# Kernel optimization log

Hardware: AMD Instinct MI355X
Metric: run time of the kernel (lower is better)

Reference implementation:

```python
import jax, jax.numpy as jnp
import numpy as np

HIDDEN = 1024
N_HEADS = 16
D_HEAD = HIDDEN // N_HEADS


def _rope(q, k):
    # q, k: [B, H, N, d]; interleaved-pair rotation as in the torch module
    B, H, N, d = q.shape
    inv_freq = 1.0 / (10000.0 ** (jnp.arange(0, d, 2, dtype=jnp.float32) / d))  # [d/2]
    pos = jnp.arange(N, dtype=jnp.float32)
    thetas = pos[:, None] * inv_freq[None, :]            # [N, d/2]
    cos, sin = jnp.cos(thetas), jnp.sin(thetas)

    def rot(x):
        xp = x.reshape(B, H, N, d // 2, 2)
        xx, xy = xp[..., 0], xp[..., 1]
        rx = xx * cos - xy * sin
        ry = xx * sin + xy * cos
        return jnp.stack([rx, ry], axis=-1).reshape(B, H, N, d)

    return rot(q), rot(k)


def setup_inputs() -> dict:
    key = jax.random.key(0)
    ks = jax.random.split(key, 9)
    B, N, Hd = 4, 2048, HIDDEN
    s = 1.0 / np.sqrt(Hd)
    return {
        "x": jax.random.normal(ks[0], (B, N, Hd), jnp.float32),
        "Wq": jax.random.normal(ks[1], (Hd, Hd), jnp.float32) * s,
        "bq": jax.random.normal(ks[2], (Hd,), jnp.float32) * 0.02,
        "Wk": jax.random.normal(ks[3], (Hd, Hd), jnp.float32) * s,
        "bk": jax.random.normal(ks[4], (Hd,), jnp.float32) * 0.02,
        "Wv": jax.random.normal(ks[5], (Hd, Hd), jnp.float32) * s,
        "bv": jax.random.normal(ks[6], (Hd,), jnp.float32) * 0.02,
        "Wo": jax.random.normal(ks[7], (Hd, Hd), jnp.float32) * s,
        "bo": jax.random.normal(ks[8], (Hd,), jnp.float32) * 0.02,
    }


def reference(x, Wq, bq, Wk, bk, Wv, bv, Wo, bo):
    B, N, _ = x.shape
    H, d = N_HEADS, D_HEAD
    # torch nn.Linear: y = x @ W.T + b
    q = (x @ Wq.T + bq).reshape(B, N, H, d).transpose(0, 2, 1, 3)  # [B,H,N,d]
    k = (x @ Wk.T + bk).reshape(B, N, H, d).transpose(0, 2, 1, 3)
    v = (x @ Wv.T + bv).reshape(B, N, H, d).transpose(0, 2, 1, 3)
    q, k = _rope(q, k)
    scores = jnp.einsum("bhnd,bhmd->bhnm", q, k) / jnp.sqrt(jnp.asarray(d, x.dtype))
    attn = jax.nn.softmax(scores, axis=-1)
    out = jnp.einsum("bhnm,bhmd->bhnd", attn, v)
    out = out.transpose(0, 2, 1, 3).reshape(B, N, H * d)
    return out @ Wo.T + bo
```

## Files before the change

### kernel.cpp

```cpp
#include <hip/hip_runtime.h>
#include <cmath>

typedef unsigned short u16;
typedef unsigned int u32;
typedef __bf16 bf16_t;
typedef bf16_t bf16x8 __attribute__((ext_vector_type(8)));
typedef float f32x4 __attribute__((ext_vector_type(4)));
typedef u32 u32x4 __attribute__((ext_vector_type(4)));

#define AS1 __attribute__((address_space(1)))
#define AS3 __attribute__((address_space(3)))

__device__ __forceinline__ void g2l16(const void* g, void* l) {
  __builtin_amdgcn_global_load_lds((const AS1 void*)g, (AS3 void*)l, 16, 0, 0);
}

__device__ __forceinline__ u16 f2b(float f) {
  u32 u = __builtin_bit_cast(u32, f);
  u += 0x7FFFu + ((u >> 16) & 1u);
  return (u16)(u >> 16);
}
__device__ __forceinline__ float b2f(u16 h) {
  u32 u = ((u32)h) << 16;
  return __builtin_bit_cast(float, u);
}

__device__ __forceinline__ float exp2fast(float x) {
#if __has_builtin(__builtin_amdgcn_exp2f)
  return __builtin_amdgcn_exp2f(x);
#else
  return exp2f(x);
#endif
}

__device__ __forceinline__ u32 cvtpk(float lo, float hi) {
  u32 d;
  asm("v_cvt_pk_bf16_f32 %0, %1, %2" : "=v"(d) : "v"(lo), "v"(hi));
  return d;
}

__global__ void mha_f2b_kernel(const float* __restrict__ in, u16* __restrict__ out, int n4) {
  int i = blockIdx.x * blockDim.x + threadIdx.x;
  if (i >= n4) return;
  float4 f = reinterpret_cast<const float4*>(in)[i];
  ushort4 o;
  o.x = f2b(f.x); o.y = f2b(f.y); o.z = f2b(f.z); o.w = f2b(f.w);
  reinterpret_cast<ushort4*>(out)[i] = o;
}

__global__ void mha_f2b4_kernel(const float* __restrict__ a0, const float* __restrict__ a1,
                                const float* __restrict__ a2, const float* __restrict__ a3,
                                u16* __restrict__ o0, u16* __restrict__ o1,
                                u16* __restrict__ o2, u16* __restrict__ o3, int n4) {
  int y = blockIdx.y;
  const float* in = y == 0 ? a0 : y == 1 ? a1 : y == 2 ? a2 : a3;
  u16* out = y == 0 ? o0 : y == 1 ? o1 : y == 2 ? o2 : o3;
  int i = blockIdx.x * blockDim.x + threadIdx.x;
  if (i >= n4) return;
  float4 f = reinterpret_cast<const float4*>(in)[i];
  ushort4 o;
  o.x = f2b(f.x); o.y = f2b(f.y); o.z = f2b(f.z); o.w = f2b(f.w);
  reinterpret_cast<ushort4*>(out)[i] = o;
}

#define BM 128
#define BN 128
#define BK 32

__global__ __launch_bounds__(256) void mha_gemm_bt(
    const u16* __restrict__ A, const u16* __restrict__ Bm,
    const float* __restrict__ bias,
    float* __restrict__ Cf, u16* __restrict__ Cb,
    int M, int N, int K)
{
  __shared__ u16 As[BM * BK];
  __shared__ u16 Bs[BN * BK];
  const int tid = threadIdx.x;
  const int wid = tid >> 6, lane = tid & 63;
  const int r16 = lane & 15, g = lane >> 4;
  const int bm = blockIdx.x * BM, bn = blockIdx.y * BN;
  const int wm = (wid >> 1) * 64, wn = (wid & 1) * 64;

  f32x4 acc[4][4] = {};

  const int srow = tid >> 2;
  const int sbyte = (tid & 3) * 16;

  for (int kt = 0; kt < K; kt += BK) {
#pragma unroll
    for (int p = 0; p < 2; ++p) {
      int ra = p * 64 + srow;
      int csw = (sbyte ^ ((ra & 3) << 4)) >> 1;
      g2l16(A  + (size_t)(bm + ra) * K + kt + csw, (u16*)As + p * 2048 + wid * 512);
      g2l16(Bm + (size_t)(bn + ra) * K + kt + csw, (u16*)Bs + p * 2048 + wid * 512);
    }
    __syncthreads();
    bf16x8 af[4], bfr[4];
#pragma unroll
    for (int mf = 0; mf < 4; ++mf) {
      int rr = wm + mf * 16 + r16;
      af[mf] = *reinterpret_cast<const bf16x8*>(&As[rr * 32 + ((g * 8) ^ ((rr & 3) << 3))]);
    }
#pragma unroll
    for (int nf = 0; nf < 4; ++nf) {
      int rr = wn + nf * 16 + r16;
      bfr[nf] = *reinterpret_cast<const bf16x8*>(&Bs[rr * 32 + ((g * 8) ^ ((rr & 3) << 3))]);
    }
    __builtin_amdgcn_s_setprio(1);
#pragma unroll
    for (int mf = 0; mf < 4; ++mf)
#pragma unroll
      for (int nf = 0; nf < 4; ++nf)
        acc[mf][nf] = __builtin_amdgcn_mfma_f32_16x16x32_bf16(af[mf], bfr[nf], acc[mf][nf], 0, 0, 0);
    __builtin_amdgcn_s_setprio(0);
    __syncthreads();
  }

#pragma unroll
  for (int mf = 0; mf < 4; ++mf)
#pragma unroll
    for (int nf = 0; nf < 4; ++nf) {
      int col = bn + wn + nf * 16 + r16;
      float bv = bias ? bias[col] : 0.f;
#pragma unroll
      for (int r = 0; r < 4; ++r) {
        int rowm = bm + wm + mf * 16 + g * 4 + r;
        float v = acc[mf][nf][r] + bv;
        if (Cf) Cf[(size_t)rowm * N + col] = v;
        else    Cb[(size_t)rowm * N + col] = f2b(v);
      }
    }
}

__global__ __launch_bounds__(256) void mha_gemm_qkv(
    const u16* __restrict__ A,
    const u16* __restrict__ W0, const u16* __restrict__ W1, const u16* __restrict__ W2,
    const float* __restrict__ b0, const float* __restrict__ b1, const float* __restrict__ b2,
    u16* __restrict__ C0, u16* __restrict__ C1, u16* __restrict__ C2,
    int M, int N, int K)
{
  __shared__ u16 As[BM * BK];
  __shared__ u16 Bs[BN * BK];
  const int tid = threadIdx.x;
  const int wid = tid >> 6, lane = tid & 63;
  const int r16 = lane & 15, g = lane >> 4;
  const int by = blockIdx.y;
  const int wsel = by >> 3;
  const u16* Bm = wsel == 0 ? W0 : (wsel == 1 ? W1 : W2);
  const float* bias = wsel == 0 ? b0 : (wsel == 1 ? b1 : b2);
  u16* Cb = wsel == 0 ? C0 : (wsel == 1 ? C1 : C2);
  const int bm = blockIdx.x * BM, bn = (by & 7) * BN;
  const int wm = (wid >> 1) * 64, wn = (wid & 1) * 64;

  f32x4 acc[4][4] = {};

  const int srow = tid >> 2;
  const int sbyte = (tid & 3) * 16;

  for (int kt = 0; kt < K; kt += BK) {
#pragma unroll
    for (int p = 0; p < 2; ++p) {
      int ra = p * 64 + srow;
      int csw = (sbyte ^ ((ra & 3) << 4)) >> 1;
      g2l16(A  + (size_t)(bm + ra) * K + kt + csw, (u16*)As + p * 2048 + wid * 512);
      g2l16(Bm + (size_t)(bn + ra) * K + kt + csw, (u16*)Bs + p * 2048 + wid * 512);
    }
    __syncthreads();
    bf16x8 af[4], bfr[4];
#pragma unroll
    for (int mf = 0; mf < 4; ++mf) {
      int rr = wm + mf * 16 + r16;
      af[mf] = *reinterpret_cast<const bf16x8*>(&As[rr * 32 + ((g * 8) ^ ((rr & 3) << 3))]);
    }
#pragma unroll
    for (int nf = 0; nf < 4; ++nf) {
      int rr = wn + nf * 16 + r16;
      bfr[nf] = *reinterpret_cast<const bf16x8*>(&Bs[rr * 32 + ((g * 8) ^ ((rr & 3) << 3))]);
    }
    __builtin_amdgcn_s_setprio(1);
#pragma unroll
    for (int mf = 0; mf < 4; ++mf)
#pragma unroll
      for (int nf = 0; nf < 4; ++nf)
        acc[mf][nf] = __builtin_amdgcn_mfma_f32_16x16x32_bf16(af[mf], bfr[nf], acc[mf][nf], 0, 0, 0);
    __builtin_amdgcn_s_setprio(0);
    __syncthreads();
  }

#pragma unroll
  for (int mf = 0; mf < 4; ++mf)
#pragma unroll
    for (int nf = 0; nf < 4; ++nf) {
      int col = bn + wn + nf * 16 + r16;
      float bv = bias[col];
#pragma unroll
      for (int r = 0; r < 4; ++r) {
        int rowm = bm + wm + mf * 16 + g * 4 + r;
        Cb[(size_t)rowm * N + col] = f2b(acc[mf][nf][r] + bv);
      }
    }
}

__global__ void mha_rope_kernel(u16* __restrict__ Q, u16* __restrict__ Kt) {
  int idx = blockIdx.x * blockDim.x + threadIdx.x;
  u16* P = blockIdx.y ? Kt : Q;
  int rowp = idx >> 9;
  int pc = idx & 511;
  int n = rowp & 2047;
  int j = pc & 31;
  float inv = exp2f(-(float)j * 0.41524101186092503f);
  float th = (float)n * inv;
  float s, c;
  sincosf(th, &s, &c);
  u32* p32 = reinterpret_cast<u32*>(P + (size_t)rowp * 1024 + pc * 2);
  u32 v = *p32;
  float x = b2f((u16)(v & 0xFFFFu));
  float y = b2f((u16)(v >> 16));
  float rx = x * c - y * s;
  float ry = x * s + y * c;
  *p32 = (u32)f2b(rx) | ((u32)f2b(ry) << 16);
}

__global__ void mha_vtrans_kernel(const u16* __restrict__ V, u16* __restrict__ Vt) {
  __shared__ u16 t[64][65];
  const int bh = blockIdx.y;
  const int b = bh >> 4, h = bh & 15;
  const int n0 = blockIdx.x * 64;
  const int tid = threadIdx.x;
#pragma unroll
  for (int i = 0; i < 2; ++i) {
    int rr = i * 32 + (tid >> 3);
    int c8 = (tid & 7) * 8;
    uint4 w = *reinterpret_cast<const uint4*>(V + (size_t)(b * 2048 + n0 + rr) * 1024 + h * 64 + c8);
    t[rr][c8 + 0] = (u16)(w.x & 0xFFFFu); t[rr][c8 + 1] = (u16)(w.x >> 16);
    t[rr][c8 + 2] = (u16)(w.y & 0xFFFFu); t[rr][c8 + 3] = (u16)(w.y >> 16);
    t[rr][c8 + 4] = (u16)(w.z & 0xFFFFu); t[rr][c8 + 5] = (u16)(w.z >> 16);
    t[rr][c8 + 6] = (u16)(w.w & 0xFFFFu); t[rr][c8 + 7] = (u16)(w.w >> 16);
  }
  __syncthreads();
#pragma unroll
  for (int i = 0; i < 2; ++i) {
    int dd = i * 32 + (tid >> 3);
    int nn8 = (tid & 7) * 8;
    u32 w0 = (u32)t[nn8 + 0][dd] | ((u32)t[nn8 + 1][dd] << 16);
    u32 w1 = (u32)t[nn8 + 2][dd] | ((u32)t[nn8 + 3][dd] << 16);
    u32 w2 = (u32)t[nn8 + 4][dd] | ((u32)t[nn8 + 5][dd] << 16);
    u32 w3 = (u32)t[nn8 + 6][dd] | ((u32)t[nn8 + 7][dd] << 16);
    uint4 w{w0, w1, w2, w3};
    *reinterpret_cast<uint4*>(Vt + (size_t)(bh * 64 + dd) * 2048 + n0 + nn8) = w;
  }
}

#define QT 256
#define KVT 128
#define NKV 16

__global__ __launch_bounds__(512) void mha_attn_kernel(
    const u16* __restrict__ Q, const u16* __restrict__ Kmat,
    const u16* __restrict__ Vt, u16* __restrict__ Ao)
{
  __shared__ u16 Ks[2][KVT * 64];
  __shared__ u16 Vs[2][64 * KVT];
  const int tid = threadIdx.x;
  const int wid = tid >> 6, lane = tid & 63;
  const int r16 = lane & 15, g = lane >> 4;
  const int bh = blockIdx.x;
  const int b = bh >> 4, h = bh & 15;
  const int q0 = blockIdx.y * QT;
  const int wr = wid * 32;

  bf16x8 qf[2][2];
#pragma unroll
  for (int qb = 0; qb < 2; ++qb)
#pragma unroll
    for (int c = 0; c < 2; ++c)
      qf[qb][c] = *reinterpret_cast<const bf16x8*>(
          Q + (size_t)(b * 2048 + q0 + wr + qb * 16 + r16) * 1024 + h * 64 + c * 32 + g * 8);

  f32x4 accO[2][4] = {};
  float mrow[2] = {-INFINITY, -INFINITY};
  float lrow[2] = {0.f, 0.f};
  const float C = 0.18033688011111793f;

  const int rk = tid >> 3, cbk = (tid & 7) * 16;
  const int rv = tid >> 4, cbv = (tid & 15) * 16;

  auto STAGE = [&](int buf, int j0) {
#pragma unroll
    for (int p = 0; p < 2; ++p) {
      int rr = p * 64 + rk;
      int csw = (cbk ^ ((rr & 7) << 4)) >> 1;
      g2l16(Kmat + (size_t)(b * 2048 + j0 + rr) * 1024 + h * 64 + csw,
            (u16*)Ks[buf] + p * 4096 + wid * 512);
    }
#pragma unroll
    for (int p = 0; p < 2; ++p) {
      int dd = p * 32 + rv;
      int csw = (cbv ^ ((dd & 7) << 4)) >> 1;
      g2l16(Vt + (size_t)(bh * 64 + dd) * 2048 + j0 + csw,
            (u16*)Vs[buf] + p * 4096 + wid * 512);
    }
  };

  STAGE(0, 0);
  __syncthreads();

  for (int t = 0; t < NKV; ++t) {
    const int cur = t & 1;
    if (t + 1 < NKV) STAGE(cur ^ 1, (t + 1) * KVT);

    f32x4 s[2][8] = {};
    const u16* KsC = Ks[cur];
#pragma unroll
    for (int c = 0; c < 2; ++c) {
      bf16x8 kf[8];
#pragma unroll
      for (int nf = 0; nf < 8; ++nf) {
        int rr = nf * 16 + r16;
        int ob = (c * 64 + g * 16) ^ ((rr & 7) << 4);
        kf[nf] = *reinterpret_cast<const bf16x8*>(&KsC[rr * 64 + (ob >> 1)]);
      }
      __builtin_amdgcn_s_setprio(1);
#pragma unroll
      for (int qb = 0; qb < 2; ++qb)
#pragma unroll
        for (int nf = 0; nf < 8; ++nf)
          s[qb][nf] = __builtin_amdgcn_mfma_f32_16x16x32_bf16(kf[nf], qf[qb][c], s[qb][nf], 0, 0, 0);
      __builtin_amdgcn_s_setprio(0);
    }

#pragma unroll
    for (int qb = 0; qb < 2; ++qb) {
      float mx = s[qb][0][0];
#pragma unroll
      for (int nf = 0; nf < 8; ++nf)
#pragma unroll
        for (int r = 0; r < 4; ++r)
          mx = fmaxf(mx, s[qb][nf][r]);
      mx = fmaxf(mx, __shfl_xor(mx, 16));
      mx = fmaxf(mx, __shfl_xor(mx, 32));
      if (!__all(mx - mrow[qb] <= 64.f)) {
        float mn = fmaxf(mrow[qb], mx);
        float corr = exp2fast((mrow[qb] - mn) * C);
        mrow[qb] = mn;
        lrow[qb] *= corr;
#pragma unroll
        for (int r = 0; r < 4; ++r) {
          float cb = __shfl(corr, g * 4 + r);
#pragma unroll
          for (int nf = 0; nf < 4; ++nf) accO[qb][nf][r] *= cb;
        }
      }
      float nb = mrow[qb] * C;
      float rs = 0.f;
#pragma unroll
      for (int nf = 0; nf < 8; ++nf)
#pragma unroll
        for (int r = 0; r < 4; ++r) {
          float p = exp2fast(fmaf(s[qb][nf][r], C, -nb));
          s[qb][nf][r] = p;
          rs += p;
        }
      rs += __shfl_xor(rs, 16);
      rs += __shfl_xor(rs, 32);
      lrow[qb] += rs;
    }

    bf16x8 pa[2][4];
#pragma unroll
    for (int qb = 0; qb < 2; ++qb)
#pragma unroll
      for (int ks = 0; ks < 4; ++ks) {
        u32 X0 = cvtpk(s[qb][2 * ks][0], s[qb][2 * ks][1]);
        u32 X1 = cvtpk(s[qb][2 * ks][2], s[qb][2 * ks][3]);
        u32 Y0 = cvtpk(s[qb][2 * ks + 1][0], s[qb][2 * ks + 1][1]);
        u32 Y1 = cvtpk(s[qb][2 * ks + 1][2], s[qb][2 * ks + 1][3]);
        asm("v_permlane32_swap_b32 %0, %1" : "+v"(X0), "+v"(Y0));
        asm("v_permlane16_swap_b32 %0, %1" : "+v"(X0), "+v"(Y0));
        asm("v_permlane32_swap_b32 %0, %1" : "+v"(X1), "+v"(Y1));
        asm("v_permlane16_swap_b32 %0, %1" : "+v"(X1), "+v"(Y1));
        u32x4 w = {X0, X1, Y0, Y1};
        pa[qb][ks] = __builtin_bit_cast(bf16x8, w);
      }

    const u16* VsC = Vs[cur];
#pragma unroll
    for (int ks = 0; ks < 4; ++ks) {
      bf16x8 vb[4];
#pragma unroll
      for (int nf = 0; nf < 4; ++nf) {
        int dd = nf * 16 + r16;
        int ob = (ks * 64 + g * 16) ^ ((dd & 7) << 4);
        vb[nf] = *reinterpret_cast<const bf16x8*>(&VsC[dd * 128 + (ob >> 1)]);
      }
      __builtin_amdgcn_s_setprio(1);
#pragma unroll
      for (int qb = 0; qb < 2; ++qb)
#pragma unroll
        for (int nf = 0; nf < 4; ++nf)
          accO[qb][nf] = __builtin_amdgcn_mfma_f32_16x16x32_bf16(pa[qb][ks], vb[nf], accO[qb][nf], 0, 0, 0);
      __builtin_amdgcn_s_setprio(0);
    }
    __syncthreads();
  }

#pragma unroll
  for (int qb = 0; qb < 2; ++qb) {
    float linv = 1.f / lrow[qb];
#pragma unroll
    for (int r = 0; r < 4; ++r) {
      float lb = __shfl(linv, g * 4 + r);
      int rowm = q0 + wr + qb * 16 + g * 4 + r;
#pragma unroll
      for (int nf = 0; nf < 4; ++nf) {
        int dd = nf * 16 + r16;
        Ao[(size_t)(b * 2048 + rowm) * 1024 + h * 64 + dd] = f2b(accO[qb][nf][r] * lb);
      }
    }
  }
}

extern "C" void kernel_launch(void* const* d_in, const int* in_sizes, int n_in,
                              void* d_out, int out_size, void* d_ws, size_t ws_size,
                              hipStream_t stream)
{
  const float* x  = (const float*)d_in[0];
  const float* Wq = (const float*)d_in[1];
  const float* bq = (const float*)d_in[2];
  const float* Wk = (const float*)d_in[3];
  const float* bk = (const float*)d_in[4];
  const float* Wv = (const float*)d_in[5];
  const float* bv = (const float*)d_in[6];
  const float* Wo = (const float*)d_in[7];
  const float* bo = (const float*)d_in[8];
  float* out = (float*)d_out;

  char* ws = (char*)d_ws;
  u16* xb  = (u16*)(ws + 0);
  u16* Wqb = (u16*)(ws + 16777216);
  u16* Wkb = (u16*)(ws + 18874368);
  u16* Wvb = (u16*)(ws + 20971520);
  u16* Wob = (u16*)(ws + 23068672);
  u16* Qb  = (u16*)(ws + 25165824);
  u16* Kb  = (u16*)(ws + 41943040);
  u16* Vb  = (u16*)(ws + 58720256);
  u16* Vtb = (u16*)(ws + 75497472);
  u16* Ab  = (u16*)(ws + 92274688);

  mha_f2b_kernel<<<8192, 256, 0, stream>>>(x, xb, 2097152);
  mha_f2b4_kernel<<<dim3(1024, 4), 256, 0, stream>>>(Wq, Wk, Wv, Wo, Wqb, Wkb, Wvb, Wob, 262144);

  mha_gemm_qkv<<<dim3(64, 24), 256, 0, stream>>>(xb, Wqb, Wkb, Wvb, bq, bk, bv,
                                                 Qb, Kb, Vb, 8192, 1024, 1024);

  mha_rope_kernel<<<dim3(16384, 2), 256, 0, stream>>>(Qb, Kb);
  mha_vtrans_kernel<<<dim3(32, 64), 256, 0, stream>>>(Vb, Vtb);

  mha_attn_kernel<<<dim3(64, 8), 512, 0, stream>>>(Qb, Kb, Vtb, Ab);

  mha_gemm_bt<<<dim3(64, 8), 256, 0, stream>>>(Ab, Wob, bo, out, nullptr, 8192, 1024, 1024);
}
```

Measured before the change: 233.2 us.

## Fuse RoPE and V transpose into QKV GEMM epilogue; row sums via MFMA

The QKV GEMM epilogue now applies the rotary embedding to Q and K in registers, using a lane shuffle to fetch the paired element and hardware sin/cos on revolutions. It also writes V directly in transposed layout, which removes the separate rope and transpose kernels and their extra global round-trips. In the attention kernel, the softmax row sums are computed by an extra MFMA against a ones vector instead of a VALU sum plus cross-lane shuffles, and the max reduction becomes a tree. The cost is more epilogue arithmetic, uncoalesced 8-byte transposed stores for V, and hardware sin/cos precision.

```diff
diff --git a/kernel.cpp b/kernel.cpp
--- a/kernel.cpp
+++ b/kernel.cpp
@@ -30,6 +30,21 @@
   return __builtin_amdgcn_exp2f(x);
 #else
   return exp2f(x);
+#endif
+}
+
+__device__ __forceinline__ float sin01(float rev) {
+#if __has_builtin(__builtin_amdgcn_sinf)
+  return __builtin_amdgcn_sinf(rev);
+#else
+  return __sinf(rev * 6.283185307179586f);
+#endif
+}
+__device__ __forceinline__ float cos01(float rev) {
+#if __has_builtin(__builtin_amdgcn_cosf)
+  return __builtin_amdgcn_cosf(rev);
+#else
+  return __cosf(rev * 6.283185307179586f);
 #endif
 }
 
@@ -70,7 +85,7 @@
 __global__ __launch_bounds__(256) void mha_gemm_bt(
     const u16* __restrict__ A, const u16* __restrict__ Bm,
     const float* __restrict__ bias,
-    float* __restrict__ Cf, u16* __restrict__ Cb,
+    float* __restrict__ Cf,
     int M, int N, int K)
 {
   __shared__ u16 As[BM * BK];
@@ -121,13 +136,11 @@
 #pragma unroll
     for (int nf = 0; nf < 4; ++nf) {
       int col = bn + wn + nf * 16 + r16;
-      float bv = bias ? bias[col] : 0.f;
+      float bv = bias[col];
 #pragma unroll
       for (int r = 0; r < 4; ++r) {
         int rowm = bm + wm + mf * 16 + g * 4 + r;
-        float v = acc[mf][nf][r] + bv;
-        if (Cf) Cf[(size_t)rowm * N + col] = v;
-        else    Cb[(size_t)rowm * N + col] = f2b(v);
+        Cf[(size_t)rowm * N + col] = acc[mf][nf][r] + bv;
       }
     }
 }
@@ -136,7 +149,7 @@
     const u16* __restrict__ A,
     const u16* __restrict__ W0, const u16* __restrict__ W1, const u16* __restrict__ W2,
     const float* __restrict__ b0, const float* __restrict__ b1, const float* __restrict__ b2,
-    u16* __restrict__ C0, u16* __restrict__ C1, u16* __restrict__ C2,
+    u16* __restrict__ C0, u16* __restrict__ C1, u16* __restrict__ Vt,
     int M, int N, int K)
 {
   __shared__ u16 As[BM * BK];
@@ -148,7 +161,6 @@
   const int wsel = by >> 3;
   const u16* Bm = wsel == 0 ? W0 : (wsel == 1 ? W1 : W2);
   const float* bias = wsel == 0 ? b0 : (wsel == 1 ? b1 : b2);
-  u16* Cb = wsel == 0 ? C0 : (wsel == 1 ? C1 : C2);
   const int bm = blockIdx.x * BM, bn = (by & 7) * BN;
   const int wm = (wid >> 1) * 64, wn = (wid & 1) * 64;
 
@@ -187,67 +199,52 @@
     __syncthreads();
   }
 
-#pragma unroll
-  for (int mf = 0; mf < 4; ++mf)
+  if (wsel == 2) {
+#pragma unroll
+    for (int mf = 0; mf < 4; ++mf) {
+      int rowbase = bm + wm + mf * 16 + g * 4;
+      int bb = rowbase >> 11;
+      int nb = rowbase & 2047;
+#pragma unroll
+      for (int nf = 0; nf < 4; ++nf) {
+        int col = bn + wn + nf * 16 + r16;
+        float bv = bias[col];
+        int hh = col >> 6, dd = col & 63;
+        u16 w0 = f2b(acc[mf][nf][0] + bv);
+        u16 w1 = f2b(acc[mf][nf][1] + bv);
+        u16 w2 = f2b(acc[mf][nf][2] + bv);
+        u16 w3 = f2b(acc[mf][nf][3] + bv);
+        uint2 pkt;
+        pkt.x = (u32)w0 | ((u32)w1 << 16);
+        pkt.y = (u32)w2 | ((u32)w3 << 16);
+        *reinterpret_cast<uint2*>(Vt + ((size_t)((bb * 16 + hh) * 64 + dd)) * 2048 + nb) = pkt;
+      }
+    }
+  } else {
+    u16* Cb = wsel == 0 ? C0 : C1;
 #pragma unroll
     for (int nf = 0; nf < 4; ++nf) {
       int col = bn + wn + nf * 16 + r16;
       float bv = bias[col];
-#pragma unroll
-      for (int r = 0; r < 4; ++r) {
-        int rowm = bm + wm + mf * 16 + g * 4 + r;
-        Cb[(size_t)rowm * N + col] = f2b(acc[mf][nf][r] + bv);
-      }
-    }
-}
-
-__global__ void mha_rope_kernel(u16* __restrict__ Q, u16* __restrict__ Kt) {
-  int idx = blockIdx.x * blockDim.x + threadIdx.x;
-  u16* P = blockIdx.y ? Kt : Q;
-  int rowp = idx >> 9;
-  int pc = idx & 511;
-  int n = rowp & 2047;
-  int j = pc & 31;
-  float inv = exp2f(-(float)j * 0.41524101186092503f);
-  float th = (float)n * inv;
-  float s, c;
-  sincosf(th, &s, &c);
-  u32* p32 = reinterpret_cast<u32*>(P + (size_t)rowp * 1024 + pc * 2);
-  u32 v = *p32;
-  float x = b2f((u16)(v & 0xFFFFu));
-  float y = b2f((u16)(v >> 16));
-  float rx = x * c - y * s;
-  float ry = x * s + y * c;
-  *p32 = (u32)f2b(rx) | ((u32)f2b(ry) << 16);
-}
-
-__global__ void mha_vtrans_kernel(const u16* __restrict__ V, u16* __restrict__ Vt) {
-  __shared__ u16 t[64][65];
-  const int bh = blockIdx.y;
-  const int b = bh >> 4, h = bh & 15;
-  const int n0 = blockIdx.x * 64;
-  const int tid = threadIdx.x;
-#pragma unroll
-  for (int i = 0; i < 2; ++i) {
-    int rr = i * 32 + (tid >> 3);
-    int c8 = (tid & 7) * 8;
-    uint4 w = *reinterpret_cast<const uint4*>(V + (size_t)(b * 2048 + n0 + rr) * 1024 + h * 64 + c8);
-    t[rr][c8 + 0] = (u16)(w.x & 0xFFFFu); t[rr][c8 + 1] = (u16)(w.x >> 16);
-    t[rr][c8 + 2] = (u16)(w.y & 0xFFFFu); t[rr][c8 + 3] = (u16)(w.y >> 16);
-    t[rr][c8 + 4] = (u16)(w.z & 0xFFFFu); t[rr][c8 + 5] = (u16)(w.z >> 16);
-    t[rr][c8 + 6] = (u16)(w.w & 0xFFFFu); t[rr][c8 + 7] = (u16)(w.w >> 16);
-  }
-  __syncthreads();
-#pragma unroll
-  for (int i = 0; i < 2; ++i) {
-    int dd = i * 32 + (tid >> 3);
-    int nn8 = (tid & 7) * 8;
-    u32 w0 = (u32)t[nn8 + 0][dd] | ((u32)t[nn8 + 1][dd] << 16);
-    u32 w1 = (u32)t[nn8 + 2][dd] | ((u32)t[nn8 + 3][dd] << 16);
-    u32 w2 = (u32)t[nn8 + 4][dd] | ((u32)t[nn8 + 5][dd] << 16);
-    u32 w3 = (u32)t[nn8 + 6][dd] | ((u32)t[nn8 + 7][dd] << 16);
-    uint4 w{w0, w1, w2, w3};
-    *reinterpret_cast<uint4*>(Vt + (size_t)(bh * 64 + dd) * 2048 + n0 + nn8) = w;
+      int j = (nf * 16 + r16) >> 1;
+      float invj = exp2f(-(float)j * 0.41524101186092503f);
+      float invrev = invj * 0.15915494309189535f;
+#pragma unroll
+      for (int mf = 0; mf < 4; ++mf) {
+#pragma unroll
+        for (int r = 0; r < 4; ++r) {
+          int rowm = bm + wm + mf * 16 + g * 4 + r;
+          float v = acc[mf][nf][r] + bv;
+          float pv = __shfl_xor(v, 1);
+          float rev = (float)(rowm & 2047) * invrev;
+          rev -= floorf(rev);
+          float sn = sin01(rev), cs = cos01(rev);
+          float tt = pv * sn;
+          float res = fmaf(v, cs, (r16 & 1) ? tt : -tt);
+          Cb[(size_t)rowm * N + col] = f2b(res);
+        }
+      }
+    }
   }
 }
 
@@ -269,6 +266,9 @@
   const int q0 = blockIdx.y * QT;
   const int wr = wid * 32;
 
+  const u32x4 onesw = {0x3F803F80u, 0x3F803F80u, 0x3F803F80u, 0x3F803F80u};
+  const bf16x8 onesf = __builtin_bit_cast(bf16x8, onesw);
+
   bf16x8 qf[2][2];
 #pragma unroll
   for (int qb = 0; qb < 2; ++qb)
@@ -278,8 +278,8 @@
           Q + (size_t)(b * 2048 + q0 + wr + qb * 16 + r16) * 1024 + h * 64 + c * 32 + g * 8);
 
   f32x4 accO[2][4] = {};
+  f32x4 accL[2] = {};
   float mrow[2] = {-INFINITY, -INFINITY};
-  float lrow[2] = {0.f, 0.f};
   const float C = 0.18033688011111793f;
 
   const int rk = tid >> 3, cbk = (tid & 7) * 16;
@@ -331,39 +331,36 @@
 
 #pragma unroll
     for (int qb = 0; qb < 2; ++qb) {
-      float mx = s[qb][0][0];
-#pragma unroll
-      for (int nf = 0; nf < 8; ++nf)
-#pragma unroll
-        for (int r = 0; r < 4; ++r)
-          mx = fmaxf(mx, s[qb][nf][r]);
+      float t0[4];
+#pragma unroll
+      for (int r = 0; r < 4; ++r) {
+        float a = fmaxf(s[qb][0][r], s[qb][1][r]);
+        float bmx = fmaxf(s[qb][2][r], s[qb][3][r]);
+        float cmx = fmaxf(s[qb][4][r], s[qb][5][r]);
+        float dmx = fmaxf(s[qb][6][r], s[qb][7][r]);
+        t0[r] = fmaxf(fmaxf(a, bmx), fmaxf(cmx, dmx));
+      }
+      float mx = fmaxf(fmaxf(t0[0], t0[1]), fmaxf(t0[2], t0[3]));
       mx = fmaxf(mx, __shfl_xor(mx, 16));
       mx = fmaxf(mx, __shfl_xor(mx, 32));
       if (!__all(mx - mrow[qb] <= 64.f)) {
         float mn = fmaxf(mrow[qb], mx);
         float corr = exp2fast((mrow[qb] - mn) * C);
         mrow[qb] = mn;
-        lrow[qb] *= corr;
 #pragma unroll
         for (int r = 0; r < 4; ++r) {
           float cb = __shfl(corr, g * 4 + r);
 #pragma unroll
           for (int nf = 0; nf < 4; ++nf) accO[qb][nf][r] *= cb;
+          accL[qb][r] *= cb;
         }
       }
       float nb = mrow[qb] * C;
-      float rs = 0.f;
 #pragma unroll
       for (int nf = 0; nf < 8; ++nf)
 #pragma unroll
-        for (int r = 0; r < 4; ++r) {
-          float p = exp2fast(fmaf(s[qb][nf][r], C, -nb));
-          s[qb][nf][r] = p;
-          rs += p;
-        }
-      rs += __shfl_xor(rs, 16);
-      rs += __shfl_xor(rs, 32);
-      lrow[qb] += rs;
+        for (int r = 0; r < 4; ++r)
+          s[qb][nf][r] = exp2fast(fmaf(s[qb][nf][r], C, -nb));
     }
 
     bf16x8 pa[2][4];
@@ -395,10 +392,12 @@
       }
       __builtin_amdgcn_s_setprio(1);
 #pragma unroll
-      for (int qb = 0; qb < 2; ++qb)
+      for (int qb = 0; qb < 2; ++qb) {
 #pragma unroll
         for (int nf = 0; nf < 4; ++nf)
           accO[qb][nf] = __builtin_amdgcn_mfma_f32_16x16x32_bf16(pa[qb][ks], vb[nf], accO[qb][nf], 0, 0, 0);
+        accL[qb] = __builtin_amdgcn_mfma_f32_16x16x32_bf16(pa[qb][ks], onesf, accL[qb], 0, 0, 0);
+      }
       __builtin_amdgcn_s_setprio(0);
     }
     __syncthreads();
@@ -406,10 +405,9 @@
 
 #pragma unroll
   for (int qb = 0; qb < 2; ++qb) {
-    float linv = 1.f / lrow[qb];
 #pragma unroll
     for (int r = 0; r < 4; ++r) {
-      float lb = __shfl(linv, g * 4 + r);
+      float lb = 1.f / accL[qb][r];
       int rowm = q0 + wr + qb * 16 + g * 4 + r;
 #pragma unroll
       for (int nf = 0; nf < 4; ++nf) {
@@ -443,20 +441,16 @@
   u16* Wob = (u16*)(ws + 23068672);
   u16* Qb  = (u16*)(ws + 25165824);
   u16* Kb  = (u16*)(ws + 41943040);
-  u16* Vb  = (u16*)(ws + 58720256);
-  u16* Vtb = (u16*)(ws + 75497472);
-  u16* Ab  = (u16*)(ws + 92274688);
+  u16* Vtb = (u16*)(ws + 58720256);
+  u16* Ab  = (u16*)(ws + 75497472);
 
   mha_f2b_kernel<<<8192, 256, 0, stream>>>(x, xb, 2097152);
   mha_f2b4_kernel<<<dim3(1024, 4), 256, 0, stream>>>(Wq, Wk, Wv, Wo, Wqb, Wkb, Wvb, Wob, 262144);
 
   mha_gemm_qkv<<<dim3(64, 24), 256, 0, stream>>>(xb, Wqb, Wkb, Wvb, bq, bk, bv,
-                                                 Qb, Kb, Vb, 8192, 1024, 1024);
-
-  mha_rope_kernel<<<dim3(16384, 2), 256, 0, stream>>>(Qb, Kb);
-  mha_vtrans_kernel<<<dim3(32, 64), 256, 0, stream>>>(Vb, Vtb);
+                                                 Qb, Kb, Vtb, 8192, 1024, 1024);
 
   mha_attn_kernel<<<dim3(64, 8), 512, 0, stream>>>(Qb, Kb, Vtb, Ab);
 
-  mha_gemm_bt<<<dim3(64, 8), 256, 0, stream>>>(Ab, Wob, bo, out, nullptr, 8192, 1024, 1024);
-}
+  mha_gemm_bt<<<dim3(64, 8), 256, 0, stream>>>(Ab, Wob, bo, out, 8192, 1024, 1024);
+}
```

Result: no change. 230.1 us (-1.3%).
